# Performance work log

Measured on AMD Instinct MI355X. Metric: run time of the kernel, lower is better.

Reference implementation:

```python
import jax, jax.numpy as jnp
import numpy as np


def setup_inputs() -> dict:
    key = jax.random.key(0)
    k1, k2, k3 = jax.random.split(key, 3)
    C, N, M = 16, 192, 16
    scale = 1.0 / C ** 2
    x = jax.random.normal(k1, (C, N, N, N), dtype=jnp.float32)
    wr = jax.random.uniform(k2, (4, C, C, M, M, M), minval=-scale, maxval=scale, dtype=jnp.float32)
    wi = jax.random.uniform(k3, (4, C, C, M, M, M), minval=-scale, maxval=scale, dtype=jnp.float32)
    return {"x": x, "wr": wr, "wi": wi, "modes": M}


def _mix(w, xf):
    # w: (Cin, Cout, m, m, m) complex; xf: (Cin, m, m, m) complex -> (Cout, m, m, m)
    return jnp.einsum('ixyz,ioxyz->oxyz', xf, w)


def reference(x, wr, wi, modes):
    m = modes
    spatial = x.shape[1:]
    # Forward real FFT over the 3 spatial axes: (C, N, N, N//2+1) complex
    xf = jnp.fft.rfftn(x, axes=(1, 2, 3))
    w = (wr + 1j * wi).astype(xf.dtype)  # (4, Cin, Cout, m, m, m)
    out_fs = jnp.zeros_like(xf)
    # Four low-frequency corner blocks (standard FNO-3D mode truncation)
    out_fs = out_fs.at[:, :m, :m, :m].set(_mix(w[0], xf[:, :m, :m, :m]))
    out_fs = out_fs.at[:, -m:, :m, :m].set(_mix(w[1], xf[:, -m:, :m, :m]))
    out_fs = out_fs.at[:, :m, -m:, :m].set(_mix(w[2], xf[:, :m, -m:, :m]))
    out_fs = out_fs.at[:, -m:, -m:, :m].set(_mix(w[3], xf[:, -m:, -m:, :m]))
    # Inverse real FFT back to physical space
    return jnp.fft.irfftn(out_fs, s=spatial, axes=(1, 2, 3))
```

## Files before the change

kernel.cpp:

```cpp
#include <hip/hip_runtime.h>
#include <math.h>


#define NN 192
#define NC 16
#define NM 16
#define NK2 32

constexpr float TWOPI  = 6.283185307179586476925286766559f;
constexpr float INV_N3 = 1.0f / (192.0f * 192.0f * 192.0f);

__device__ __forceinline__ void fill_T(float2* T) {
  int t = threadIdx.x;
  if (t < NN) {
    float s, c;
    sincosf((TWOPI / NN) * (float)t, &s, &c);
    T[t] = make_float2(c, s);
  }
}

__global__ __launch_bounds__(256) void k1_fwd_z(const float* __restrict__ x,
                                                float2* __restrict__ A) {
  __shared__ float xs[64 * 193];
  __shared__ float2 T[NN];
  const int t = threadIdx.x;
  fill_T(T);
  const int rowBase = blockIdx.x * 64;
  const float4* src = (const float4*)(x + (size_t)rowBase * NN);
#pragma unroll
  for (int k = 0; k < 12; ++k) {
    int i = t + k * 256;
    float4 v = src[i];
    int fi = i << 2;
    int row = fi / NN;
    int z = fi - row * NN;
    float* d = &xs[row * 193 + z];
    d[0] = v.x; d[1] = v.y; d[2] = v.z; d[3] = v.w;
  }
  __syncthreads();
  const int kz = t & 15;
  const int r0 = (t >> 4) << 2;
  float ar[4] = {0.f, 0.f, 0.f, 0.f};
  float ai[4] = {0.f, 0.f, 0.f, 0.f};
  int p = 0;
#pragma unroll 8
  for (int z = 0; z < NN; ++z) {
    float2 w = T[p];
    p += kz; p = (p >= NN) ? p - NN : p;
#pragma unroll
    for (int r = 0; r < 4; ++r) {
      float xv = xs[(r0 + r) * 193 + z];
      ar[r] = fmaf(xv, w.x, ar[r]);
      ai[r] = fmaf(-xv, w.y, ai[r]);
    }
  }
  float2* dst = A + (size_t)rowBase * NM;
#pragma unroll
  for (int r = 0; r < 4; ++r)
    dst[(r0 + r) * NM + kz] = make_float2(ar[r], ai[r]);
}

__global__ __launch_bounds__(256) void k2_fwd_y(const float2* __restrict__ A,
                                                float2* __restrict__ B) {
  __shared__ __align__(16) float2 As[NN * NM];
  __shared__ float2 T[NN];
  const int t = threadIdx.x;
  fill_T(T);
  const int cx = blockIdx.x;
  const float4* src = (const float4*)(A + (size_t)cx * NN * NM);
  float4* dl = (float4*)As;
#pragma unroll
  for (int k = 0; k < 6; ++k) dl[t + k * 256] = src[t + k * 256];
  __syncthreads();
  const int kz = t & 15;
  const int kyq = t >> 4;
  const int s1 = 176 + kyq;
  float2 a0 = make_float2(0.f, 0.f), a1 = make_float2(0.f, 0.f);
  int p0 = 0, p1 = 0;
#pragma unroll 4
  for (int y = 0; y < NN; ++y) {
    float2 a = As[y * NM + kz];
    float2 w0 = T[p0]; p0 += kyq; p0 = (p0 >= NN) ? p0 - NN : p0;
    float2 w1 = T[p1]; p1 += s1;  p1 = (p1 >= NN) ? p1 - NN : p1;
    a0.x = fmaf(a.x, w0.x, fmaf(a.y, w0.y, a0.x));
    a0.y = fmaf(a.y, w0.x, fmaf(-a.x, w0.y, a0.y));
    a1.x = fmaf(a.x, w1.x, fmaf(a.y, w1.y, a1.x));
    a1.y = fmaf(a.y, w1.x, fmaf(-a.x, w1.y, a1.y));
  }
  float2* dst = B + (size_t)cx * NK2 * NM;
  dst[kyq * NM + kz] = a0;
  dst[(16 + kyq) * NM + kz] = a1;
}

__global__ __launch_bounds__(256) void k3_fwd_x(const float2* __restrict__ B,
                                                float2* __restrict__ Xf) {
  __shared__ __align__(16) float2 Bs[NN * NM];
  __shared__ float2 T[NN];
  const int t = threadIdx.x;
  fill_T(T);
  const int c = blockIdx.x >> 5, ky = blockIdx.x & 31;
#pragma unroll
  for (int k = 0; k < 6; ++k) {
    int i = t + k * 256;
    int xx = i >> 3, q = i & 7;
    ((float4*)Bs)[i] = *((const float4*)(B + ((size_t)(c * NN + xx) * NK2 + ky) * NM) + q);
  }
  __syncthreads();
  const int kz = t & 15, kxq = t >> 4;
  const int s1 = 176 + kxq;
  float2 a0 = make_float2(0.f, 0.f), a1 = make_float2(0.f, 0.f);
  int p0 = 0, p1 = 0;
#pragma unroll 4
  for (int xx = 0; xx < NN; ++xx) {
    float2 b = Bs[xx * NM + kz];
    float2 w0 = T[p0]; p0 += kxq; p0 = (p0 >= NN) ? p0 - NN : p0;
    float2 w1 = T[p1]; p1 += s1;  p1 = (p1 >= NN) ? p1 - NN : p1;
    a0.x = fmaf(b.x, w0.x, fmaf(b.y, w0.y, a0.x));
    a0.y = fmaf(b.y, w0.x, fmaf(-b.x, w0.y, a0.y));
    a1.x = fmaf(b.x, w1.x, fmaf(b.y, w1.y, a1.x));
    a1.y = fmaf(b.y, w1.x, fmaf(-b.x, w1.y, a1.y));
  }
  Xf[((size_t)(c * NK2 + kxq) * NK2 + ky) * NM + kz] = a0;
  Xf[((size_t)(c * NK2 + 16 + kxq) * NK2 + ky) * NM + kz] = a1;
}

__global__ __launch_bounds__(256) void k4_mix(const float2* __restrict__ Xf,
                                              const float* __restrict__ wr,
                                              const float* __restrict__ wi,
                                              float2* __restrict__ Y) {
  const int tm = blockIdx.x * 256 + threadIdx.x;
  const int kz = tm & 15, ky = (tm >> 4) & 31, kx = tm >> 9;
  const int q = (kx >= 16 ? 1 : 0) + (ky >= 16 ? 2 : 0);
  const int modeW = ((kx & 15) * 16 + (ky & 15)) * 16 + kz;
  float xr[NC], xi[NC];
#pragma unroll
  for (int i = 0; i < NC; ++i) {
    float2 v = Xf[i * 16384 + tm];
    xr[i] = v.x; xi[i] = v.y;
  }
  const float scale = (kz == 0 ? 1.0f : 2.0f) * INV_N3;
#pragma unroll 1
  for (int o = 0; o < NC; ++o) {
    float cr = 0.f, ci = 0.f;
#pragma unroll
    for (int i = 0; i < NC; ++i) {
      size_t wIdx = (size_t)((q * 16 + i) * 16 + o) * 4096 + modeW;
      float a = wr[wIdx], b = wi[wIdx];
      cr = fmaf(xr[i], a, fmaf(-xi[i], b, cr));
      ci = fmaf(xr[i], b, fmaf(xi[i], a, ci));
    }
    Y[o * 16384 + tm] = make_float2(cr * scale, ci * scale);
  }
}

__global__ __launch_bounds__(256) void k5_inv_x(const float2* __restrict__ Y,
                                                float2* __restrict__ G1) {
  __shared__ __align__(16) float2 Ys[NK2 * NM];
  __shared__ float2 T[NN];
  const int t = threadIdx.x;
  fill_T(T);
  const int c = blockIdx.x >> 5, ky = blockIdx.x & 31;
  {
    int kx = t >> 3, qq = t & 7;
    ((float4*)Ys)[t] = *((const float4*)(Y + (size_t)c * 16384 + (size_t)kx * (NK2 * NM) + ky * NM) + qq);
  }
  __syncthreads();
  const int kz = t & 15, xq = t >> 4;
#pragma unroll 1
  for (int j = 0; j < 12; ++j) {
    const int xx = xq + 16 * j;
    float2 acc = make_float2(0.f, 0.f);
    const int step = xx;
    int p = 0;
#pragma unroll
    for (int k = 0; k < 16; ++k) {
      float2 v = Ys[k * NM + kz];
      float2 w = T[p]; p += step; p = (p >= NN) ? p - NN : p;
      acc.x = fmaf(v.x, w.x, fmaf(-v.y, w.y, acc.x));
      acc.y = fmaf(v.y, w.x, fmaf( v.x, w.y, acc.y));
    }
    int p2 = (176 * xx) % NN;
#pragma unroll
    for (int k = 0; k < 16; ++k) {
      float2 v = Ys[(16 + k) * NM + kz];
      float2 w = T[p2]; p2 += step; p2 = (p2 >= NN) ? p2 - NN : p2;
      acc.x = fmaf(v.x, w.x, fmaf(-v.y, w.y, acc.x));
      acc.y = fmaf(v.y, w.x, fmaf( v.x, w.y, acc.y));
    }
    G1[((size_t)(c * NN + xx) * NK2 + ky) * NM + kz] = acc;
  }
}

__global__ __launch_bounds__(256) void k6_inv_y(const float2* __restrict__ G1,
                                                float2* __restrict__ G2) {
  __shared__ __align__(16) float2 Gs[NK2 * NM];
  __shared__ float2 T[NN];
  const int t = threadIdx.x;
  fill_T(T);
  const int cx = blockIdx.x;
  ((float4*)Gs)[t] = ((const float4*)(G1 + (size_t)cx * NK2 * NM))[t];
  __syncthreads();
  const int kz = t & 15, yq = t >> 4;
#pragma unroll 1
  for (int j = 0; j < 12; ++j) {
    const int y = yq + 16 * j;
    float2 acc = make_float2(0.f, 0.f);
    const int step = y;
    int p = 0;
#pragma unroll
    for (int k = 0; k < 16; ++k) {
      float2 v = Gs[k * NM + kz];
      float2 w = T[p]; p += step; p = (p >= NN) ? p - NN : p;
      acc.x = fmaf(v.x, w.x, fmaf(-v.y, w.y, acc.x));
      acc.y = fmaf(v.y, w.x, fmaf( v.x, w.y, acc.y));
    }
    int p2 = (176 * y) % NN;
#pragma unroll
    for (int k = 0; k < 16; ++k) {
      float2 v = Gs[(16 + k) * NM + kz];
      float2 w = T[p2]; p2 += step; p2 = (p2 >= NN) ? p2 - NN : p2;
      acc.x = fmaf(v.x, w.x, fmaf(-v.y, w.y, acc.x));
      acc.y = fmaf(v.y, w.x, fmaf( v.x, w.y, acc.y));
    }
    G2[((size_t)cx * NN + y) * NM + kz] = acc;
  }
}

__global__ __launch_bounds__(192) void k7_inv_z(const float2* __restrict__ G2,
                                                float* __restrict__ out) {
  __shared__ __align__(16) float2 Gs[NN * NM];
  __shared__ float2 T[NN];
  const int t = threadIdx.x;
  fill_T(T);
  const int cx = blockIdx.x;
  const float4* src = (const float4*)(G2 + (size_t)cx * NN * NM);
#pragma unroll
  for (int k = 0; k < 8; ++k) ((float4*)Gs)[t + k * 192] = src[t + k * 192];
  __syncthreads();
  const int z = t;
  float twc[16], tws[16];
#pragma unroll
  for (int kz = 0; kz < 16; ++kz) {
    float2 w = T[(kz * z) % NN];
    twc[kz] = w.x; tws[kz] = w.y;
  }
  const float4* Gs4 = (const float4*)Gs;
  float* obase = out + (size_t)cx * NN * NN;
#pragma unroll 2
  for (int y = 0; y < NN; ++y) {
    float acc = 0.f;
#pragma unroll
    for (int h = 0; h < 8; ++h) {
      float4 g = Gs4[y * 8 + h];
      acc = fmaf(g.x, twc[2 * h],     fmaf(-g.y, tws[2 * h],     acc));
      acc = fmaf(g.z, twc[2 * h + 1], fmaf(-g.w, tws[2 * h + 1], acc));
    }
    obase[y * NN + z] = acc;
  }
}

extern "C" void kernel_launch(void* const* d_in, const int* in_sizes, int n_in,
                              void* d_out, int out_size, void* d_ws, size_t ws_size,
                              hipStream_t stream) {
  const float* x  = (const float*)d_in[0];
  const float* wr = (const float*)d_in[1];
  const float* wi = (const float*)d_in[2];
  float* out = (float*)d_out;

  float2* A  = (float2*)d_ws;
  float2* B  = A  + 9437184;
  float2* Xf = B  + 1572864;
  float2* Y  = Xf + 262144;
  float2* G1 = B;
  float2* G2 = A;

  k1_fwd_z<<<dim3(9216), dim3(256), 0, stream>>>(x, A);
  k2_fwd_y<<<dim3(3072), dim3(256), 0, stream>>>(A, B);
  k3_fwd_x<<<dim3(512),  dim3(256), 0, stream>>>(B, Xf);
  k4_mix  <<<dim3(64),   dim3(256), 0, stream>>>(Xf, wr, wi, Y);
  k5_inv_x<<<dim3(512),  dim3(256), 0, stream>>>(Y, G1);
  k6_inv_y<<<dim3(3072), dim3(256), 0, stream>>>(G1, G2);
  k7_inv_z<<<dim3(3072), dim3(192), 0, stream>>>(G2, out);
}
```

Before: 1.121 ms.

## Precompute twiddle tables and restructure forward-z, mix, inverse-y and inverse-z kernels

Adds two small kernels that precompute twiddle tables in global memory (T1 for the forward z DFT, T32 for the inverse y/z DFTs), replacing per-block sincos setup and shared-memory twiddle indexing. k1 becomes one-thread-per-row, reading x directly with float4 loads and accumulating all 16 modes in registers. k4 spreads output channels across blocks, raising the grid from 64 to 1024 blocks. k6 and k7 drop shared-memory staging and read from global and cache instead. The aim is to cut shared-memory traffic and increase parallelism, at the cost of uncoalesced per-thread row reads in k1 and higher register pressure.

```diff
diff --git a/kernel.cpp b/kernel.cpp
--- a/kernel.cpp
+++ b/kernel.cpp
@@ -19,45 +19,53 @@
   }
 }
 
+__global__ __launch_bounds__(256) void k0a_t1(float2* __restrict__ T1) {
+  int idx = blockIdx.x * 256 + threadIdx.x;
+  int z = idx >> 4, kz = idx & 15;
+  float s, c;
+  sincosf((TWOPI / NN) * (float)((z * kz) % NN), &s, &c);
+  T1[idx] = make_float2(c, -s);
+}
+
+__global__ __launch_bounds__(256) void k0b_t32(float2* __restrict__ T32) {
+  int idx = blockIdx.x * 256 + threadIdx.x;
+  int f = idx >> 5, j = idx & 31;
+  int freq = (j < 16) ? j : (160 + j);
+  float s, c;
+  sincosf((TWOPI / NN) * (float)((f * freq) % NN), &s, &c);
+  T32[idx] = make_float2(c, s);
+}
+
 __global__ __launch_bounds__(256) void k1_fwd_z(const float* __restrict__ x,
+                                                const float2* __restrict__ T1,
                                                 float2* __restrict__ A) {
-  __shared__ float xs[64 * 193];
-  __shared__ float2 T[NN];
-  const int t = threadIdx.x;
-  fill_T(T);
-  const int rowBase = blockIdx.x * 64;
-  const float4* src = (const float4*)(x + (size_t)rowBase * NN);
-#pragma unroll
-  for (int k = 0; k < 12; ++k) {
-    int i = t + k * 256;
-    float4 v = src[i];
-    int fi = i << 2;
-    int row = fi / NN;
-    int z = fi - row * NN;
-    float* d = &xs[row * 193 + z];
-    d[0] = v.x; d[1] = v.y; d[2] = v.z; d[3] = v.w;
-  }
-  __syncthreads();
-  const int kz = t & 15;
-  const int r0 = (t >> 4) << 2;
-  float ar[4] = {0.f, 0.f, 0.f, 0.f};
-  float ai[4] = {0.f, 0.f, 0.f, 0.f};
-  int p = 0;
-#pragma unroll 8
-  for (int z = 0; z < NN; ++z) {
-    float2 w = T[p];
-    p += kz; p = (p >= NN) ? p - NN : p;
-#pragma unroll
-    for (int r = 0; r < 4; ++r) {
-      float xv = xs[(r0 + r) * 193 + z];
-      ar[r] = fmaf(xv, w.x, ar[r]);
-      ai[r] = fmaf(-xv, w.y, ai[r]);
-    }
-  }
-  float2* dst = A + (size_t)rowBase * NM;
-#pragma unroll
-  for (int r = 0; r < 4; ++r)
-    dst[(r0 + r) * NM + kz] = make_float2(ar[r], ai[r]);
+  const int r = blockIdx.x * 256 + threadIdx.x;
+  const float* __restrict__ xr = x + (size_t)r * NN;
+  float ar[NM], ai[NM];
+#pragma unroll
+  for (int k = 0; k < NM; ++k) { ar[k] = 0.f; ai[k] = 0.f; }
+#pragma unroll 1
+  for (int zc = 0; zc < 12; ++zc) {
+    float4 v[4];
+    const float4* src = (const float4*)(xr + zc * 16);
+#pragma unroll
+    for (int q = 0; q < 4; ++q) v[q] = src[q];
+#pragma unroll
+    for (int zz = 0; zz < 16; ++zz) {
+      const float xv = ((const float*)v)[zz];
+      const float2* tz = T1 + (zc * 16 + zz) * NM;
+#pragma unroll
+      for (int kz = 0; kz < NM; ++kz) {
+        float2 w = tz[kz];
+        ar[kz] = fmaf(xv, w.x, ar[kz]);
+        ai[kz] = fmaf(xv, w.y, ai[kz]);
+      }
+    }
+  }
+  float4* dst = (float4*)(A + (size_t)r * NM);
+#pragma unroll
+  for (int h = 0; h < 8; ++h)
+    dst[h] = make_float4(ar[2 * h], ai[2 * h], ar[2 * h + 1], ai[2 * h + 1]);
 }
 
 __global__ __launch_bounds__(256) void k2_fwd_y(const float2* __restrict__ A,
@@ -128,29 +136,23 @@
                                               const float* __restrict__ wr,
                                               const float* __restrict__ wi,
                                               float2* __restrict__ Y) {
-  const int tm = blockIdx.x * 256 + threadIdx.x;
+  const int o  = blockIdx.x & 15;
+  const int mc = blockIdx.x >> 4;
+  const int tm = mc * 256 + threadIdx.x;
   const int kz = tm & 15, ky = (tm >> 4) & 31, kx = tm >> 9;
   const int q = (kx >= 16 ? 1 : 0) + (ky >= 16 ? 2 : 0);
   const int modeW = ((kx & 15) * 16 + (ky & 15)) * 16 + kz;
-  float xr[NC], xi[NC];
+  float cr = 0.f, ci = 0.f;
 #pragma unroll
   for (int i = 0; i < NC; ++i) {
     float2 v = Xf[i * 16384 + tm];
-    xr[i] = v.x; xi[i] = v.y;
+    size_t wIdx = (size_t)((q * 16 + i) * 16 + o) * 4096 + modeW;
+    float a = wr[wIdx], b = wi[wIdx];
+    cr = fmaf(v.x, a, fmaf(-v.y, b, cr));
+    ci = fmaf(v.x, b, fmaf(v.y, a, ci));
   }
   const float scale = (kz == 0 ? 1.0f : 2.0f) * INV_N3;
-#pragma unroll 1
-  for (int o = 0; o < NC; ++o) {
-    float cr = 0.f, ci = 0.f;
-#pragma unroll
-    for (int i = 0; i < NC; ++i) {
-      size_t wIdx = (size_t)((q * 16 + i) * 16 + o) * 4096 + modeW;
-      float a = wr[wIdx], b = wi[wIdx];
-      cr = fmaf(xr[i], a, fmaf(-xi[i], b, cr));
-      ci = fmaf(xr[i], b, fmaf(xi[i], a, ci));
-    }
-    Y[o * 16384 + tm] = make_float2(cr * scale, ci * scale);
-  }
+  Y[o * 16384 + tm] = make_float2(cr * scale, ci * scale);
 }
 
 __global__ __launch_bounds__(256) void k5_inv_x(const float2* __restrict__ Y,
@@ -192,68 +194,61 @@
 }
 
 __global__ __launch_bounds__(256) void k6_inv_y(const float2* __restrict__ G1,
+                                                const float2* __restrict__ T32,
                                                 float2* __restrict__ G2) {
-  __shared__ __align__(16) float2 Gs[NK2 * NM];
-  __shared__ float2 T[NN];
-  const int t = threadIdx.x;
-  fill_T(T);
+  const int t = threadIdx.x;
+  const int kz = t & 15, xi = t >> 4;
+  const int ys = blockIdx.x & 3;
+  const int g  = blockIdx.x >> 2;
+  const int c  = g / 12, xg = g - c * 12;
+  const int x  = xg * 16 + xi;
+  const size_t cx = (size_t)(c * NN + x);
+  float gr[NK2], gi[NK2];
+  const float2* __restrict__ src = G1 + cx * NK2 * NM + kz;
+#pragma unroll
+  for (int k = 0; k < NK2; ++k) {
+    float2 v = src[k * NM];
+    gr[k] = v.x; gi[k] = v.y;
+  }
+  float2* dst = G2 + cx * NN * NM + kz;
+  const int y0 = ys * 48;
+#pragma unroll 1
+  for (int y = y0; y < y0 + 48; ++y) {
+    const float2* tw = T32 + y * NK2;
+    float sr = 0.f, si = 0.f;
+#pragma unroll
+    for (int k = 0; k < NK2; ++k) {
+      float2 w = tw[k];
+      sr = fmaf(gr[k], w.x, fmaf(-gi[k], w.y, sr));
+      si = fmaf(gi[k], w.x, fmaf( gr[k], w.y, si));
+    }
+    dst[y * NM] = make_float2(sr, si);
+  }
+}
+
+__global__ __launch_bounds__(192) void k7_inv_z(const float2* __restrict__ G2,
+                                                const float2* __restrict__ T32,
+                                                float* __restrict__ out) {
+  const int z = threadIdx.x;
   const int cx = blockIdx.x;
-  ((float4*)Gs)[t] = ((const float4*)(G1 + (size_t)cx * NK2 * NM))[t];
-  __syncthreads();
-  const int kz = t & 15, yq = t >> 4;
-#pragma unroll 1
-  for (int j = 0; j < 12; ++j) {
-    const int y = yq + 16 * j;
-    float2 acc = make_float2(0.f, 0.f);
-    const int step = y;
-    int p = 0;
-#pragma unroll
-    for (int k = 0; k < 16; ++k) {
-      float2 v = Gs[k * NM + kz];
-      float2 w = T[p]; p += step; p = (p >= NN) ? p - NN : p;
-      acc.x = fmaf(v.x, w.x, fmaf(-v.y, w.y, acc.x));
-      acc.y = fmaf(v.y, w.x, fmaf( v.x, w.y, acc.y));
-    }
-    int p2 = (176 * y) % NN;
-#pragma unroll
-    for (int k = 0; k < 16; ++k) {
-      float2 v = Gs[(16 + k) * NM + kz];
-      float2 w = T[p2]; p2 += step; p2 = (p2 >= NN) ? p2 - NN : p2;
-      acc.x = fmaf(v.x, w.x, fmaf(-v.y, w.y, acc.x));
-      acc.y = fmaf(v.y, w.x, fmaf( v.x, w.y, acc.y));
-    }
-    G2[((size_t)cx * NN + y) * NM + kz] = acc;
-  }
-}
-
-__global__ __launch_bounds__(192) void k7_inv_z(const float2* __restrict__ G2,
-                                                float* __restrict__ out) {
-  __shared__ __align__(16) float2 Gs[NN * NM];
-  __shared__ float2 T[NN];
-  const int t = threadIdx.x;
-  fill_T(T);
-  const int cx = blockIdx.x;
-  const float4* src = (const float4*)(G2 + (size_t)cx * NN * NM);
-#pragma unroll
-  for (int k = 0; k < 8; ++k) ((float4*)Gs)[t + k * 192] = src[t + k * 192];
-  __syncthreads();
-  const int z = t;
   float twc[16], tws[16];
-#pragma unroll
-  for (int kz = 0; kz < 16; ++kz) {
-    float2 w = T[(kz * z) % NN];
-    twc[kz] = w.x; tws[kz] = w.y;
-  }
-  const float4* Gs4 = (const float4*)Gs;
+  const float4* tz = (const float4*)(T32 + (size_t)z * NK2);
+#pragma unroll
+  for (int h = 0; h < 8; ++h) {
+    float4 w = tz[h];
+    twc[2 * h]     = w.x; tws[2 * h]     = w.y;
+    twc[2 * h + 1] = w.z; tws[2 * h + 1] = w.w;
+  }
+  const float2* __restrict__ gbase = G2 + (size_t)cx * NN * NM;
   float* obase = out + (size_t)cx * NN * NN;
 #pragma unroll 2
   for (int y = 0; y < NN; ++y) {
+    const float2* gy = gbase + y * NM;
     float acc = 0.f;
 #pragma unroll
-    for (int h = 0; h < 8; ++h) {
-      float4 g = Gs4[y * 8 + h];
-      acc = fmaf(g.x, twc[2 * h],     fmaf(-g.y, tws[2 * h],     acc));
-      acc = fmaf(g.z, twc[2 * h + 1], fmaf(-g.w, tws[2 * h + 1], acc));
+    for (int kz = 0; kz < NM; ++kz) {
+      float2 v = gy[kz];
+      acc = fmaf(v.x, twc[kz], fmaf(-v.y, tws[kz], acc));
     }
     obase[y * NN + z] = acc;
   }
@@ -273,12 +268,16 @@
   float2* Y  = Xf + 262144;
   float2* G1 = B;
   float2* G2 = A;
-
-  k1_fwd_z<<<dim3(9216), dim3(256), 0, stream>>>(x, A);
+  float2* T1  = Xf;
+  float2* T32 = Y;
+
+  k0a_t1 <<<dim3(12),   dim3(256), 0, stream>>>(T1);
+  k1_fwd_z<<<dim3(2304), dim3(256), 0, stream>>>(x, T1, A);
   k2_fwd_y<<<dim3(3072), dim3(256), 0, stream>>>(A, B);
   k3_fwd_x<<<dim3(512),  dim3(256), 0, stream>>>(B, Xf);
-  k4_mix  <<<dim3(64),   dim3(256), 0, stream>>>(Xf, wr, wi, Y);
+  k4_mix  <<<dim3(1024), dim3(256), 0, stream>>>(Xf, wr, wi, Y);
   k5_inv_x<<<dim3(512),  dim3(256), 0, stream>>>(Y, G1);
-  k6_inv_y<<<dim3(3072), dim3(256), 0, stream>>>(G1, G2);
-  k7_inv_z<<<dim3(3072), dim3(192), 0, stream>>>(G2, out);
-}
+  k0b_t32<<<dim3(24),   dim3(256), 0, stream>>>(T32);
+  k6_inv_y<<<dim3(768),  dim3(256), 0, stream>>>(G1, T32, G2);
+  k7_inv_z<<<dim3(3072), dim3(192), 0, stream>>>(G2, T32, out);
+}
```

Result: faster. 1.098 ms (-2.1%).
